# Kernel tuning notes

Measured on AMD Instinct MI355X. Metric: run time of the kernel, lower is better.

## Reference

```python
import jax, jax.numpy as jnp
import numpy as np

NUM_GRAPHS = 64
DIM = 64
NUM_FEATURES = 64
N_NODES = 5000
N_EDGES = 20000
EDGE_FEAT = 5
HID = 128  # hidden width of the edge-conditioning MLP


def setup_inputs() -> dict:
    key = jax.random.key(0)
    ks = jax.random.split(key, 20)
    d = DIM

    def unif(k, shape, fan_in):
        b = 1.0 / np.sqrt(fan_in)
        return jax.random.uniform(k, shape, jnp.float32, -b, b)

    x = jax.random.normal(ks[0], (N_NODES, NUM_FEATURES), jnp.float32)
    edge_index = jax.random.randint(ks[1], (2, N_EDGES), 0, N_NODES, jnp.int32)
    batch = jnp.sort(jax.random.randint(ks[2], (N_NODES,), 0, NUM_GRAPHS, jnp.int32))
    edge_attr = jax.random.uniform(ks[3], (N_EDGES, EDGE_FEAT), jnp.float32)

    return {
        "x": x,
        "edge_index": edge_index,
        "batch": batch,
        "edge_attr": edge_attr,
        "lin0_w": unif(ks[4], (NUM_FEATURES, d), NUM_FEATURES),
        "lin0_b": unif(ks[5], (d,), NUM_FEATURES),
        "nn_w1": unif(ks[6], (EDGE_FEAT, HID), EDGE_FEAT),
        "nn_b1": unif(ks[7], (HID,), EDGE_FEAT),
        "nn_w2": unif(ks[8], (HID, d * d), HID),
        "nn_b2": unif(ks[9], (d * d,), HID),
        "conv_b": unif(ks[10], (d,), d),
        "gru_w_ih": unif(ks[11], (3 * d, d), d),
        "gru_w_hh": unif(ks[12], (3 * d, d), d),
        "gru_b_ih": unif(ks[13], (3 * d,), d),
        "gru_b_hh": unif(ks[14], (3 * d,), d),
        "lstm_w_ih": unif(ks[15], (4 * d, 2 * d), 2 * d),
        "lstm_w_hh": unif(ks[16], (4 * d, d), d),
        "lstm_b_ih": unif(ks[17], (4 * d,), d),
        "lstm_b_hh": unif(ks[18], (4 * d,), d),
    }


def reference(x, edge_index, batch, edge_attr, lin0_w, lin0_b, nn_w1, nn_b1,
              nn_w2, nn_b2, conv_b, gru_w_ih, gru_w_hh, gru_b_ih, gru_b_hh,
              lstm_w_ih, lstm_w_hh, lstm_b_ih, lstm_b_hh):
    d = lin0_b.shape[0]
    N = x.shape[0]
    B = NUM_GRAPHS
    src, dst = edge_index[0], edge_index[1]

    out = jax.nn.relu(x @ lin0_w + lin0_b)          # [N, d]
    h = out                                         # GRU hidden state

    # Edge-conditioned weight matrices: depend only on edge_attr, compute once.
    ew = (jax.nn.relu(edge_attr @ nn_w1 + nn_b1) @ nn_w2 + nn_b2).reshape(-1, d, d)  # [E, d, d]
    deg = jnp.clip(jax.ops.segment_sum(jnp.ones(src.shape[0], x.dtype), dst,
                                       num_segments=N), 1.0)

    for _ in range(3):
        # NNConv: gather -> per-edge matvec -> scatter-mean -> bias
        msg = jnp.einsum('ei,eio->eo', out[src], ew)               # [E, d]
        agg = jax.ops.segment_sum(msg, dst, num_segments=N) / deg[:, None]
        m = jax.nn.relu(agg + conv_b)

        # Single-step GRU (torch gate order: r, z, n)
        gi = m @ gru_w_ih.T + gru_b_ih
        gh = h @ gru_w_hh.T + gru_b_hh
        ir, iz, i_n = jnp.split(gi, 3, axis=-1)
        hr, hz, h_n = jnp.split(gh, 3, axis=-1)
        r = jax.nn.sigmoid(ir + hr)
        z = jax.nn.sigmoid(iz + hz)
        n = jnp.tanh(i_n + r * h_n)
        h = (1.0 - z) * n + z * h
        out = h

    feat = out  # feat_map[-1]

    # Set2Set pooling: LSTM(2d -> d) + segment softmax attention, 3 steps
    q_star = jnp.zeros((B, 2 * d), x.dtype)
    hh = jnp.zeros((B, d), x.dtype)
    cc = jnp.zeros((B, d), x.dtype)
    for _ in range(3):
        gates = q_star @ lstm_w_ih.T + lstm_b_ih + hh @ lstm_w_hh.T + lstm_b_hh
        ii, ff, gg, oo = jnp.split(gates, 4, axis=-1)  # torch gate order i,f,g,o
        cc = jax.nn.sigmoid(ff) * cc + jax.nn.sigmoid(ii) * jnp.tanh(gg)
        hh = jax.nn.sigmoid(oo) * jnp.tanh(cc)
        q = hh
        e = jnp.sum(out * q[batch], axis=-1)                        # [N]
        e_max = jax.ops.segment_max(e, batch, num_segments=B)
        ee = jnp.exp(e - e_max[batch])
        denom = jax.ops.segment_sum(ee, batch, num_segments=B)
        a = ee / denom[batch]
        r_pool = jax.ops.segment_sum(a[:, None] * out, batch, num_segments=B)
        q_star = jnp.concatenate([q, r_pool], axis=-1)              # [B, 2d]

    return q_star, feat
```

## Files before the change

kernel.cpp:

```cpp
#include <hip/hip_runtime.h>

#define N_NODES 5000
#define N_EDGES 20000
#define B_GRAPHS 64
#define DD 64
#define HID 128
#define EDGE_FEAT 5
#define KTOT 8256
#define NTILES 258
#define NTILES_PAD 260
#define KY_SPLIT 8
#define KCHUNK 1032
#define GNB 16
#define S2SCAP 160

typedef unsigned short u16;
typedef float f32x4 __attribute__((ext_vector_type(4)));
typedef u16 u16x8 __attribute__((ext_vector_type(8)));
typedef __bf16 bf16x8 __attribute__((ext_vector_type(8)));
union AB { u16x8 u; bf16x8 b; };

__device__ __forceinline__ float b2f(u16 u) {
  union { unsigned u32; float f; } v; v.u32 = ((unsigned)u) << 16; return v.f;
}
__device__ __forceinline__ u16 f2b(float f) {
  union { float f; unsigned u; } v; v.f = f;
  unsigned r = v.u + 0x7FFF + ((v.u >> 16) & 1);
  return (u16)(r >> 16);
}
__device__ __forceinline__ float sigf(float x) { return 1.f / (1.f + expf(-x)); }

__global__ __launch_bounds__(256) void k_lin0(const float* __restrict__ x, const float* __restrict__ w,
                       const float* __restrict__ b, float* __restrict__ h) {
  __shared__ float xs[4][64];
  int wv = threadIdx.x >> 6, j = threadIdx.x & 63;
  int n = blockIdx.x * 4 + wv;
  if (n >= N_NODES) return;
  xs[wv][j] = x[(size_t)n * 64 + j];
  __syncthreads();
  float acc = b[j];
#pragma unroll
  for (int i = 0; i < 64; ++i) acc += xs[wv][i] * w[i * 64 + j];
  h[(size_t)n * 64 + j] = fmaxf(acc, 0.f);
}

__global__ void k_deg(const int* __restrict__ dst, float* __restrict__ deg) {
  int e = blockIdx.x * 256 + threadIdx.x;
  if (e < N_EDGES) atomicAdd(&deg[dst[e]], 1.0f);
}

__global__ void k_bounds(const int* __restrict__ batch, int* __restrict__ start) {
  int g = threadIdx.x;
  if (g > B_GRAPHS) return;
  int lo = 0, hi = N_NODES;
  while (lo < hi) { int mid = (lo + hi) >> 1; if (batch[mid] < g) lo = mid + 1; else hi = mid; }
  start[g] = lo;
}

__global__ __launch_bounds__(256) void k_r1b(const float* __restrict__ ea, const float* __restrict__ w1,
                      const float* __restrict__ b1, u16* __restrict__ r1,
                      const int* __restrict__ dst, float* __restrict__ deg) {
  __shared__ float a[2][EDGE_FEAT];
  int t = threadIdx.x;
  int e0 = blockIdx.x * 2;
  if (t < 2 * EDGE_FEAT) a[t / EDGE_FEAT][t % EDGE_FEAT] = ea[(size_t)e0 * EDGE_FEAT + t];
  if (t >= 32 && t < 34) atomicAdd(&deg[dst[e0 + t - 32]], 1.0f);
  __syncthreads();
  int sub = t >> 7, c = t & 127;
  float acc = b1[c];
#pragma unroll
  for (int k = 0; k < EDGE_FEAT; ++k) acc += a[sub][k] * w1[k * HID + c];
  r1[(size_t)(e0 + sub) * HID + c] = f2b(fmaxf(acc, 0.f));
}

__global__ void k_w2t2(const float* __restrict__ w2, const float* __restrict__ b2,
                       u16* __restrict__ w2tile) {
  int ks = blockIdx.x, t = threadIdx.x;
  int p0 = t * 16;
  int col = p0 >> 6;
  int rot = (p0 >> 4) & 3;
  int lkg = (rot - (col >> 1)) & 3;
  u16x8 frag;
#pragma unroll
  for (int j = 0; j < 8; ++j) {
    int kp = ks * 32 + lkg * 8 + j;
    float v = (kp < 8192) ? w2[(size_t)(kp >> 6) * 4096 + (kp & 63) * 64 + col]
                          : b2[(size_t)(kp - 8192) * 64 + col];
    frag[j] = f2b(v);
  }
  *(u16x8*)(w2tile + (size_t)ks * 2048 + t * 8) = frag;
}

__global__ __launch_bounds__(256) void k_msgf4(const int* __restrict__ src,
                                               const int* __restrict__ dst,
                                               const float* __restrict__ h,
                                               const u16* __restrict__ r1b,
                                               const u16* __restrict__ w2tile,
                                               float* __restrict__ agg) {
  __shared__ u16 r1s[64][72];
  __shared__ __align__(16) u16 Bbuf[2][8192];
  __shared__ int dsts[64];
  int bm = blockIdx.x, ky = blockIdx.y;
  int t = threadIdx.x, wave = t >> 6, lane = t & 63;

  {
    int r = t >> 2, qp = t & 3;
    int e = bm * 64 + r;
    if (t < 64) dsts[t] = (bm * 64 + t < N_EDGES) ? dst[bm * 64 + t] : -1;
    int ec = (e < N_EDGES) ? e : 0;
    const u16x8* rp = (const u16x8*)(r1b + (size_t)ec * HID + ky * 64 + qp * 16);
    *(u16x8*)&r1s[r][qp * 16] = rp[0];
    *(u16x8*)&r1s[r][qp * 16 + 8] = rp[1];
    if (qp == 0) {
      r1s[r][64] = 0x3F80;
#pragma unroll
      for (int z = 65; z < 72; ++z) r1s[r][z] = 0;
    }
  }

  int row = lane & 15, lk = (lane >> 4) * 8;
  int arow = wave * 16 + row;

  int e_a = bm * 64 + arow;
  int se = (e_a < N_EDGES) ? src[e_a] : 0;
  const float* hp = h + (size_t)se * 64;
  f32x4 ha0 = *(const f32x4*)(hp + lk);
  f32x4 ha1 = *(const f32x4*)(hp + lk + 4);
  f32x4 hb0 = *(const f32x4*)(hp + 32 + lk);
  f32x4 hb1 = *(const f32x4*)(hp + 32 + lk + 4);

  int boff[4];
#pragma unroll
  for (int ct = 0; ct < 4; ++ct) {
    int col = ct * 16 + row;
    boff[ct] = col * 32 + ((((lane >> 4) + (col >> 1)) & 3) << 3);
  }

  f32x4 acc[4];
#pragma unroll
  for (int ct = 0; ct < 4; ++ct) acc[ct] = (f32x4){0.f, 0.f, 0.f, 0.f};

  int ks0 = ky * 128;
  int nSt = ky ? 33 : 32;

  {
    size_t base = (size_t)ks0 * 2048 + t * 8;
    u16x8 q0 = *(const u16x8*)(w2tile + base);
    u16x8 q1 = *(const u16x8*)(w2tile + base + 2048);
    u16x8 q2 = *(const u16x8*)(w2tile + base + 4096);
    u16x8 q3 = *(const u16x8*)(w2tile + base + 6144);
    *(u16x8*)&Bbuf[0][t * 8] = q0;
    *(u16x8*)&Bbuf[0][2048 + t * 8] = q1;
    *(u16x8*)&Bbuf[0][4096 + t * 8] = q2;
    *(u16x8*)&Bbuf[0][6144 + t * 8] = q3;
  }
  u16x8 pv0, pv1, pv2, pv3;
  {
    size_t base = (size_t)(ks0 + 4) * 2048 + t * 8;
    pv0 = *(const u16x8*)(w2tile + base);
    pv1 = *(const u16x8*)(w2tile + base + 2048);
    pv2 = *(const u16x8*)(w2tile + base + 4096);
    pv3 = *(const u16x8*)(w2tile + base + 6144);
  }
  __syncthreads();

  for (int st = 0; st < nSt; ++st) {
    int cur = st & 1;
    if (st + 1 < nSt) {
      int nxt = cur ^ 1;
      *(u16x8*)&Bbuf[nxt][t * 8] = pv0;
      *(u16x8*)&Bbuf[nxt][2048 + t * 8] = pv1;
      *(u16x8*)&Bbuf[nxt][4096 + t * 8] = pv2;
      *(u16x8*)&Bbuf[nxt][6144 + t * 8] = pv3;
    }
    if (st + 2 < nSt) {
      size_t base = (size_t)(ks0 + (st + 2) * 4) * 2048 + t * 8;
      pv0 = *(const u16x8*)(w2tile + base);
      pv1 = *(const u16x8*)(w2tile + base + 2048);
      pv2 = *(const u16x8*)(w2tile + base + 4096);
      pv3 = *(const u16x8*)(w2tile + base + 6144);
    }
#pragma unroll
    for (int q = 0; q < 4; ++q) {
      int s = ks0 + st * 4 + q;
      int kapl = (s >> 1) - ky * 64;
      float rs = b2f(r1s[arow][kapl]);
      f32x4 h0 = (q & 1) ? hb0 : ha0;
      f32x4 h1 = (q & 1) ? hb1 : ha1;
      AB ca;
      ca.b[0] = (__bf16)(rs * h0.x); ca.b[1] = (__bf16)(rs * h0.y);
      ca.b[2] = (__bf16)(rs * h0.z); ca.b[3] = (__bf16)(rs * h0.w);
      ca.b[4] = (__bf16)(rs * h1.x); ca.b[5] = (__bf16)(rs * h1.y);
      ca.b[6] = (__bf16)(rs * h1.z); ca.b[7] = (__bf16)(rs * h1.w);
      const u16* bb = &Bbuf[cur][q * 2048];
#pragma unroll
      for (int ct = 0; ct < 4; ++ct) {
        AB cb;
        cb.u = *(const u16x8*)(bb + boff[ct]);
        acc[ct] = __builtin_amdgcn_mfma_f32_16x16x32_bf16(ca.b, cb.b, acc[ct], 0, 0, 0);
      }
    }
    __syncthreads();
  }

  int orow0 = wave * 16 + (lane >> 4) * 4;
#pragma unroll
  for (int ct = 0; ct < 4; ++ct) {
    int col = ct * 16 + row;
#pragma unroll
    for (int r = 0; r < 4; ++r) {
      int dd = dsts[orow0 + r];
      if (dd >= 0) atomicAdd(&agg[(size_t)dd * 64 + col], acc[ct][r]);
    }
  }
}

__global__ __launch_bounds__(256) void k_msgv(const int* __restrict__ src,
                                              const int* __restrict__ dst,
                                              const float* __restrict__ h,
                                              const float* __restrict__ ea,
                                              const float* __restrict__ w1,
                                              const float* __restrict__ b1,
                                              const float* __restrict__ w2,
                                              const float* __restrict__ b2,
                                              float* __restrict__ agg) {
  __shared__ float hsv[64][68];
  __shared__ float r1sv[64][132];
  __shared__ float w1s[EDGE_FEAT][HID];
  __shared__ float b1s[HID];
  __shared__ float eas[64][EDGE_FEAT];
  __shared__ int dstsv[64];

  int bm = blockIdx.x, ky = blockIdx.y;
  int t = threadIdx.x;
  int wave = t >> 6, lane = t & 63;

  if (t < HID) b1s[t] = b1[t];
  for (int i = t; i < EDGE_FEAT * HID; i += 256) w1s[i / HID][i % HID] = w1[i];
  {
    int r = t >> 2, qp = t & 3;
    int e = bm * 64 + r;
    if (t < 64) dstsv[t] = (bm * 64 + t < N_EDGES) ? dst[bm * 64 + t] : -1;
    if (e < N_EDGES) {
      int s = src[e];
#pragma unroll
      for (int i = 0; i < 16; ++i) hsv[r][qp * 16 + i] = h[(size_t)s * 64 + qp * 16 + i];
      if (qp == 0)
#pragma unroll
        for (int k = 0; k < EDGE_FEAT; ++k) eas[r][k] = ea[(size_t)e * EDGE_FEAT + k];
    } else {
#pragma unroll
      for (int i = 0; i < 16; ++i) hsv[r][qp * 16 + i] = 0.f;
      if (qp == 0)
#pragma unroll
        for (int k = 0; k < EDGE_FEAT; ++k) eas[r][k] = 0.f;
    }
  }
  __syncthreads();

  for (int idx = t; idx < 64 * HID; idx += 256) {
    int rr = idx >> 7, c = idx & 127;
    float acc = b1s[c];
#pragma unroll
    for (int k = 0; k < EDGE_FEAT; ++k) acc += eas[rr][k] * w1s[k][c];
    r1sv[rr][c] = fmaxf(acc, 0.f);
  }
  if (t < 64) r1sv[t][128] = 1.0f;
  __syncthreads();

  int row0 = wave * 16 + (lane >> 4) * 4;
  int colb = lane & 15;

  float acc[4][4];
#pragma unroll
  for (int ct = 0; ct < 4; ++ct)
#pragma unroll
    for (int r = 0; r < 4; ++r) acc[ct][r] = 0.f;

  int k0 = ky * KCHUNK, k1 = k0 + KCHUNK;
  for (int kp = k0; kp < k1; ++kp) {
    int kap = kp >> 6, ii = kp & 63;
    const float* Bp = (kp < 8192) ? (w2 + (size_t)kp * 64)
                                  : (b2 + (size_t)(kp - 8192) * 64);
    float bv[4];
#pragma unroll
    for (int ct = 0; ct < 4; ++ct) bv[ct] = Bp[ct * 16 + colb];
#pragma unroll
    for (int r = 0; r < 4; ++r) {
      float a = r1sv[row0 + r][kap] * hsv[row0 + r][ii];
#pragma unroll
      for (int ct = 0; ct < 4; ++ct) acc[ct][r] += a * bv[ct];
    }
  }

#pragma unroll
  for (int ct = 0; ct < 4; ++ct) {
    int col = ct * 16 + colb;
#pragma unroll
    for (int r = 0; r < 4; ++r) {
      int dd = dstsv[row0 + r];
      if (dd >= 0) atomicAdd(&agg[(size_t)dd * 64 + col], acc[ct][r]);
    }
  }
}

__global__ __launch_bounds__(256) void k_gru2(const float* __restrict__ agg_in, const float* __restrict__ deg,
                                              const float* __restrict__ conv_b,
                                              const float* __restrict__ wih, const float* __restrict__ whh,
                                              const float* __restrict__ bih, const float* __restrict__ bhh,
                                              float* __restrict__ h, float* __restrict__ agg_clr,
                                              float* __restrict__ outp) {
  __shared__ float ms[GNB][64], hsn[GNB][64];
  __shared__ float gis[GNB][192], ghs[GNB][192];
  int n0 = blockIdx.x * GNB;
  int t = threadIdx.x;

  for (int idx = t; idx < GNB * 64; idx += 256) {
    int r = idx >> 6, c = idx & 63;
    int n = n0 + r;
    if (n < N_NODES) {
      float dg = fmaxf(deg[n], 1.0f);
      ms[r][c] = fmaxf(agg_in[(size_t)n * 64 + c] / dg + conv_b[c], 0.f);
      hsn[r][c] = h[(size_t)n * 64 + c];
      agg_clr[(size_t)n * 64 + c] = 0.f;
    } else { ms[r][c] = 0.f; hsn[r][c] = 0.f; }
  }
  __syncthreads();

  if (t < 192) {
    f32x4 wr[16];
    const f32x4* wp = (const f32x4*)(wih + (size_t)t * 64);
#pragma unroll
    for (int i = 0; i < 16; ++i) wr[i] = wp[i];
    float bi = bih[t];
    for (int n = 0; n < GNB; ++n) {
      float acc = bi;
#pragma unroll
      for (int i = 0; i < 16; ++i) {
        f32x4 v = wr[i];
        acc += ms[n][4*i] * v.x + ms[n][4*i+1] * v.y + ms[n][4*i+2] * v.z + ms[n][4*i+3] * v.w;
      }
      gis[n][t] = acc;
    }
    const f32x4* hp2 = (const f32x4*)(whh + (size_t)t * 64);
#pragma unroll
    for (int i = 0; i < 16; ++i) wr[i] = hp2[i];
    float bh = bhh[t];
    for (int n = 0; n < GNB; ++n) {
      float acc = bh;
#pragma unroll
      for (int i = 0; i < 16; ++i) {
        f32x4 v = wr[i];
        acc += hsn[n][4*i] * v.x + hsn[n][4*i+1] * v.y + hsn[n][4*i+2] * v.z + hsn[n][4*i+3] * v.w;
      }
      ghs[n][t] = acc;
    }
  }
  __syncthreads();

  for (int idx = t; idx < GNB * 64; idx += 256) {
    int rr = idx >> 6, c = idx & 63;
    int n = n0 + rr;
    if (n < N_NODES) {
      float r = sigf(gis[rr][c] + ghs[rr][c]);
      float z = sigf(gis[rr][64 + c] + ghs[rr][64 + c]);
      float nn = tanhf(gis[rr][128 + c] + r * ghs[rr][128 + c]);
      float hv = (1.f - z) * nn + z * hsn[rr][c];
      h[(size_t)n * 64 + c] = hv;
      if (outp) outp[B_GRAPHS * 128 + (size_t)n * 64 + c] = hv;
    }
  }
}

__global__ __launch_bounds__(256) void k_s2s(const float* __restrict__ wih, const float* __restrict__ whh,
                                             const float* __restrict__ bih, const float* __restrict__ bhh,
                                             const float* __restrict__ feat, const int* __restrict__ start,
                                             float* __restrict__ ev, float* __restrict__ outq) {
  __shared__ float fl[S2SCAP][65];
  __shared__ float al[S2SCAP];
  __shared__ float qs[128], hhs[64], ccs[64], gates[256], part[4][64];
  int g = blockIdx.x, t = threadIdx.x, w = t >> 6, l = t & 63;
  int s0 = start[g], s1 = start[g + 1];
  int cnt = s1 - s0;
  bool fits = (cnt <= S2SCAP);

  if (fits) {
    for (int idx = t; idx < cnt * 16; idx += 256) {
      int n = idx >> 4, q = idx & 15;
      *(f32x4*)&fl[n][q * 4] = *(const f32x4*)(feat + (size_t)(s0 + n) * 64 + q * 4);
    }
  }
  if (t < 128) qs[t] = 0.f;
  if (t < 64) { hhs[t] = 0.f; ccs[t] = 0.f; }
  __syncthreads();

  for (int step = 0; step < 3; ++step) {
    {
      float acc = bih[t] + bhh[t];
      const f32x4* wr = (const f32x4*)(wih + (size_t)t * 128);
#pragma unroll
      for (int i = 0; i < 32; ++i) {
        f32x4 v = wr[i];
        acc += qs[4 * i] * v.x + qs[4 * i + 1] * v.y + qs[4 * i + 2] * v.z + qs[4 * i + 3] * v.w;
      }
      const f32x4* hr = (const f32x4*)(whh + (size_t)t * 64);
#pragma unroll
      for (int i = 0; i < 16; ++i) {
        f32x4 v = hr[i];
        acc += hhs[4 * i] * v.x + hhs[4 * i + 1] * v.y + hhs[4 * i + 2] * v.z + hhs[4 * i + 3] * v.w;
      }
      gates[t] = acc;
    }
    __syncthreads();
    if (t < 64) {
      float c_new = sigf(gates[64 + t]) * ccs[t] + sigf(gates[t]) * tanhf(gates[128 + t]);
      hhs[t] = sigf(gates[192 + t]) * tanhf(c_new);
      ccs[t] = c_new;
      qs[t] = hhs[t];
    }
    __syncthreads();

    float mymax = -1e30f;
    if (fits) {
      for (int n = t; n < cnt; n += 256) {
        float acc = 0.f;
#pragma unroll 16
        for (int c = 0; c < 64; ++c) acc += fl[n][c] * hhs[c];
        al[n] = acc;
        mymax = fmaxf(mymax, acc);
      }
    } else {
      for (int n = t; n < cnt; n += 256) {
        float acc = 0.f;
        for (int c = 0; c < 64; ++c) acc += feat[(size_t)(s0 + n) * 64 + c] * hhs[c];
        ev[s0 + n] = acc;
        mymax = fmaxf(mymax, acc);
      }
    }
    gates[t] = mymax; __syncthreads();
    for (int off = 128; off; off >>= 1) { if (t < off) gates[t] = fmaxf(gates[t], gates[t + off]); __syncthreads(); }
    float emax = gates[0];
    __syncthreads();

    float sd = 0.f;
    if (fits) {
      for (int n = t; n < cnt; n += 256) { float e = expf(al[n] - emax); al[n] = e; sd += e; }
    } else {
      for (int n = t; n < cnt; n += 256) sd += expf(ev[s0 + n] - emax);
    }
    gates[t] = sd; __syncthreads();
    for (int off = 128; off; off >>= 1) { if (t < off) gates[t] += gates[t + off]; __syncthreads(); }
    float den = gates[0];
    __syncthreads();

    float pacc = 0.f;
    if (fits) {
      for (int n = w; n < cnt; n += 4) pacc += al[n] * fl[n][l];
      pacc /= den;
    } else {
      for (int n = w; n < cnt; n += 4) {
        float a = expf(ev[s0 + n] - emax) / den;
        pacc += a * feat[(size_t)(s0 + n) * 64 + l];
      }
    }
    part[w][l] = pacc; __syncthreads();
    if (t < 64) qs[64 + t] = part[0][t] + part[1][t] + part[2][t] + part[3][t];
    __syncthreads();
  }
  if (t < 128) outq[g * 128 + t] = qs[t];
}

extern "C" void kernel_launch(void* const* d_in, const int* in_sizes, int n_in,
                              void* d_out, int out_size, void* d_ws, size_t ws_size,
                              hipStream_t stream) {
  (void)in_sizes; (void)n_in; (void)out_size;
  const float* x        = (const float*)d_in[0];
  const int*   ei       = (const int*)d_in[1];
  const int*   batch    = (const int*)d_in[2];
  const float* ea       = (const float*)d_in[3];
  const float* lin0_w   = (const float*)d_in[4];
  const float* lin0_b   = (const float*)d_in[5];
  const float* nn_w1    = (const float*)d_in[6];
  const float* nn_b1    = (const float*)d_in[7];
  const float* nn_w2    = (const float*)d_in[8];
  const float* nn_b2    = (const float*)d_in[9];
  const float* conv_b   = (const float*)d_in[10];
  const float* gru_w_ih = (const float*)d_in[11];
  const float* gru_w_hh = (const float*)d_in[12];
  const float* gru_b_ih = (const float*)d_in[13];
  const float* gru_b_hh = (const float*)d_in[14];
  const float* lstm_w_ih= (const float*)d_in[15];
  const float* lstm_w_hh= (const float*)d_in[16];
  const float* lstm_b_ih= (const float*)d_in[17];
  const float* lstm_b_hh= (const float*)d_in[18];
  const int* srcp = ei;
  const int* dstp = ei + N_EDGES;

  char* ws = (char*)d_ws;
  size_t off = 0;
  auto alloc = [&](size_t bytes) { void* p = ws + off; off += (bytes + 255) & ~(size_t)255; return p; };
  float* h     = (float*)alloc((size_t)N_NODES * 64 * 4);
  float* agg   = (float*)alloc((size_t)N_NODES * 64 * 4);
  float* deg   = (float*)alloc((size_t)N_NODES * 4);
  float* ev    = (float*)alloc((size_t)N_NODES * 4);
  int*   startv= (int*)alloc(65 * 4);
  u16*   r1b   = (u16*)alloc((size_t)N_EDGES * HID * 2);
  u16*   w2tile= (u16*)alloc((size_t)NTILES_PAD * 2048 * 2);
  bool useF = (ws_size >= off);

  hipMemsetAsync(deg, 0, (size_t)N_NODES * 4, stream);
  hipMemsetAsync(agg, 0, (size_t)N_NODES * 64 * 4, stream);

  k_lin0<<<(N_NODES + 3) / 4, 256, 0, stream>>>(x, lin0_w, lin0_b, h);
  k_bounds<<<1, 128, 0, stream>>>(batch, startv);

  if (useF) {
    hipMemsetAsync(w2tile + (size_t)NTILES * 2048, 0, (size_t)(NTILES_PAD - NTILES) * 2048 * 2, stream);
    k_r1b<<<N_EDGES / 2, 256, 0, stream>>>(ea, nn_w1, nn_b1, r1b, dstp, deg);
    k_w2t2<<<NTILES, 256, 0, stream>>>(nn_w2, nn_b2, w2tile);
    for (int it = 0; it < 3; ++it) {
      k_msgf4<<<dim3((N_EDGES + 63) / 64, 2), 256, 0, stream>>>(srcp, dstp, h, r1b, w2tile, agg);
      k_gru2<<<(N_NODES + GNB - 1) / GNB, 256, 0, stream>>>(agg, deg, conv_b, gru_w_ih, gru_w_hh,
                                                            gru_b_ih, gru_b_hh, h, agg,
                                                            (it == 2) ? (float*)d_out : nullptr);
    }
  } else {
    k_deg<<<(N_EDGES + 255) / 256, 256, 0, stream>>>(dstp, deg);
    for (int it = 0; it < 3; ++it) {
      k_msgv<<<dim3(313, KY_SPLIT), 256, 0, stream>>>(srcp, dstp, h, ea, nn_w1, nn_b1,
                                                      nn_w2, nn_b2, agg);
      k_gru2<<<(N_NODES + GNB - 1) / GNB, 256, 0, stream>>>(agg, deg, conv_b, gru_w_ih, gru_w_hh,
                                                            gru_b_ih, gru_b_hh, h, agg,
                                                            (it == 2) ? (float*)d_out : nullptr);
    }
  }

  k_s2s<<<B_GRAPHS, 256, 0, stream>>>(lstm_w_ih, lstm_w_hh, lstm_b_ih, lstm_b_hh,
                                      h, startv, ev, (float*)d_out);
}
```

Before: 231.2 us.

## Factor r1 scaling out of MFMA operand and split K across four blocks

The message kernel no longer builds the A operand by multiplying each hidden-unit activation r1 into h and converting to bf16 on every k-step. It precomputes bf16 h once, runs two MFMAs per hidden unit into a temporary, and scales the result by per-row r1 values in the accumulator. The K dimension is also split across four y-blocks instead of two, giving more blocks but twice as many atomic adds into agg. The per-step temporary MFMA plus vector FMA adds some latency, and rounding now applies to h alone rather than to the product r1*h.

```diff
diff --git a/kernel.cpp b/kernel.cpp
--- a/kernel.cpp
+++ b/kernel.cpp
@@ -91,13 +91,13 @@
   *(u16x8*)(w2tile + (size_t)ks * 2048 + t * 8) = frag;
 }
 
-__global__ __launch_bounds__(256) void k_msgf4(const int* __restrict__ src,
+__global__ __launch_bounds__(256) void k_msgf6(const int* __restrict__ src,
                                                const int* __restrict__ dst,
                                                const float* __restrict__ h,
                                                const u16* __restrict__ r1b,
                                                const u16* __restrict__ w2tile,
                                                float* __restrict__ agg) {
-  __shared__ u16 r1s[64][72];
+  __shared__ u16 r1s[64][40];
   __shared__ __align__(16) u16 Bbuf[2][8192];
   __shared__ int dsts[64];
   int bm = blockIdx.x, ky = blockIdx.y;
@@ -108,18 +108,20 @@
     int e = bm * 64 + r;
     if (t < 64) dsts[t] = (bm * 64 + t < N_EDGES) ? dst[bm * 64 + t] : -1;
     int ec = (e < N_EDGES) ? e : 0;
-    const u16x8* rp = (const u16x8*)(r1b + (size_t)ec * HID + ky * 64 + qp * 16);
-    *(u16x8*)&r1s[r][qp * 16] = rp[0];
-    *(u16x8*)&r1s[r][qp * 16 + 8] = rp[1];
-    if (qp == 0) {
-      r1s[r][64] = 0x3F80;
-#pragma unroll
-      for (int z = 65; z < 72; ++z) r1s[r][z] = 0;
+    if (qp < 2) {
+      const u16x8* rp = (const u16x8*)(r1b + (size_t)ec * HID + ky * 32 + qp * 16);
+      *(u16x8*)&r1s[r][qp * 16] = rp[0];
+      *(u16x8*)&r1s[r][qp * 16 + 8] = rp[1];
+    } else if (qp == 2) {
+      r1s[r][32] = (ky == 3) ? 0x3F80 : 0;
+#pragma unroll
+      for (int z = 33; z < 40; ++z) r1s[r][z] = 0;
     }
   }
 
   int row = lane & 15, lk = (lane >> 4) * 8;
   int arow = wave * 16 + row;
+  int orow0 = wave * 16 + ((lane >> 4) << 2);
 
   int e_a = bm * 64 + arow;
   int se = (e_a < N_EDGES) ? src[e_a] : 0;
@@ -128,6 +130,11 @@
   f32x4 ha1 = *(const f32x4*)(hp + lk + 4);
   f32x4 hb0 = *(const f32x4*)(hp + 32 + lk);
   f32x4 hb1 = *(const f32x4*)(hp + 32 + lk + 4);
+  AB hAb, hBb;
+  hAb.b[0] = (__bf16)ha0.x; hAb.b[1] = (__bf16)ha0.y; hAb.b[2] = (__bf16)ha0.z; hAb.b[3] = (__bf16)ha0.w;
+  hAb.b[4] = (__bf16)ha1.x; hAb.b[5] = (__bf16)ha1.y; hAb.b[6] = (__bf16)ha1.z; hAb.b[7] = (__bf16)ha1.w;
+  hBb.b[0] = (__bf16)hb0.x; hBb.b[1] = (__bf16)hb0.y; hBb.b[2] = (__bf16)hb0.z; hBb.b[3] = (__bf16)hb0.w;
+  hBb.b[4] = (__bf16)hb1.x; hBb.b[5] = (__bf16)hb1.y; hBb.b[6] = (__bf16)hb1.z; hBb.b[7] = (__bf16)hb1.w;
 
   int boff[4];
 #pragma unroll
@@ -140,8 +147,8 @@
 #pragma unroll
   for (int ct = 0; ct < 4; ++ct) acc[ct] = (f32x4){0.f, 0.f, 0.f, 0.f};
 
-  int ks0 = ky * 128;
-  int nSt = ky ? 33 : 32;
+  int ks0 = ky * 64;
+  int nSt = (ky == 3) ? 17 : 16;
 
   {
     size_t base = (size_t)ks0 * 2048 + t * 8;
@@ -181,29 +188,28 @@
       pv3 = *(const u16x8*)(w2tile + base + 6144);
     }
 #pragma unroll
-    for (int q = 0; q < 4; ++q) {
-      int s = ks0 + st * 4 + q;
-      int kapl = (s >> 1) - ky * 64;
-      float rs = b2f(r1s[arow][kapl]);
-      f32x4 h0 = (q & 1) ? hb0 : ha0;
-      f32x4 h1 = (q & 1) ? hb1 : ha1;
-      AB ca;
-      ca.b[0] = (__bf16)(rs * h0.x); ca.b[1] = (__bf16)(rs * h0.y);
-      ca.b[2] = (__bf16)(rs * h0.z); ca.b[3] = (__bf16)(rs * h0.w);
-      ca.b[4] = (__bf16)(rs * h1.x); ca.b[5] = (__bf16)(rs * h1.y);
-      ca.b[6] = (__bf16)(rs * h1.z); ca.b[7] = (__bf16)(rs * h1.w);
-      const u16* bb = &Bbuf[cur][q * 2048];
+    for (int m = 0; m < 2; ++m) {
+      int kapl = st * 2 + m;
+      f32x4 rsv;
+      rsv.x = b2f(r1s[orow0 + 0][kapl]);
+      rsv.y = b2f(r1s[orow0 + 1][kapl]);
+      rsv.z = b2f(r1s[orow0 + 2][kapl]);
+      rsv.w = b2f(r1s[orow0 + 3][kapl]);
+      const u16* bb0 = &Bbuf[cur][(2 * m) * 2048];
+      const u16* bb1 = &Bbuf[cur][(2 * m + 1) * 2048];
 #pragma unroll
       for (int ct = 0; ct < 4; ++ct) {
-        AB cb;
-        cb.u = *(const u16x8*)(bb + boff[ct]);
-        acc[ct] = __builtin_amdgcn_mfma_f32_16x16x32_bf16(ca.b, cb.b, acc[ct], 0, 0, 0);
+        AB cb0, cb1;
+        cb0.u = *(const u16x8*)(bb0 + boff[ct]);
+        cb1.u = *(const u16x8*)(bb1 + boff[ct]);
+        f32x4 P = __builtin_amdgcn_mfma_f32_16x16x32_bf16(hAb.b, cb0.b, (f32x4){0.f, 0.f, 0.f, 0.f}, 0, 0, 0);
+        P = __builtin_amdgcn_mfma_f32_16x16x32_bf16(hBb.b, cb1.b, P, 0, 0, 0);
+        acc[ct] += rsv * P;
       }
     }
     __syncthreads();
   }
 
-  int orow0 = wave * 16 + (lane >> 4) * 4;
 #pragma unroll
   for (int ct = 0; ct < 4; ++ct) {
     int col = ct * 16 + row;
@@ -519,7 +525,7 @@
     k_r1b<<<N_EDGES / 2, 256, 0, stream>>>(ea, nn_w1, nn_b1, r1b, dstp, deg);
     k_w2t2<<<NTILES, 256, 0, stream>>>(nn_w2, nn_b2, w2tile);
     for (int it = 0; it < 3; ++it) {
-      k_msgf4<<<dim3((N_EDGES + 63) / 64, 2), 256, 0, stream>>>(srcp, dstp, h, r1b, w2tile, agg);
+      k_msgf6<<<dim3((N_EDGES + 63) / 64, 4), 256, 0, stream>>>(srcp, dstp, h, r1b, w2tile, agg);
       k_gru2<<<(N_NODES + GNB - 1) / GNB, 256, 0, stream>>>(agg, deg, conv_b, gru_w_ih, gru_w_hh,
                                                             gru_b_ih, gru_b_hh, h, agg,
                                                             (it == 2) ? (float*)d_out : nullptr);
```

Result: slower. 243.3 us (+5.2%).
